# Kernel optimization log

Measured on AMD Instinct MI355X. Metric: run time of the kernel, lower is better.

The kernel has to match this reference:

```python
import jax, jax.numpy as jnp
import numpy as np

N_NODES = 100000
N_EDGES = 500000
HIDDEN = 256


def setup_inputs() -> dict:
    key = jax.random.key(0)
    k_x, k_e, k_w1, k_b1, k_w2, k_b2 = jax.random.split(key, 6)
    x = jax.random.normal(k_x, (N_NODES, HIDDEN), dtype=jnp.float32)
    edge_label_index = jax.random.randint(k_e, (2, N_EDGES), 0, N_NODES, dtype=jnp.int64)
    # fc1: Linear(2*hidden -> hidden); fc2: Linear(hidden -> 1). PyTorch stores W as [out, in].
    bound1 = 1.0 / np.sqrt(2 * HIDDEN)
    W1 = jax.random.uniform(k_w1, (HIDDEN, 2 * HIDDEN), dtype=jnp.float32, minval=-bound1, maxval=bound1)
    b1 = jax.random.uniform(k_b1, (HIDDEN,), dtype=jnp.float32, minval=-bound1, maxval=bound1)
    bound2 = 1.0 / np.sqrt(HIDDEN)
    W2 = jax.random.uniform(k_w2, (1, HIDDEN), dtype=jnp.float32, minval=-bound2, maxval=bound2)
    b2 = jax.random.uniform(k_b2, (1,), dtype=jnp.float32, minval=-bound2, maxval=bound2)
    return {"x": x, "edge_label_index": edge_label_index, "W1": W1, "b1": b1, "W2": W2, "b2": b2}


def reference(x, edge_label_index, W1, b1, W2, b2):
    # Gather endpoint features: [E, H] each
    feat_src = x[edge_label_index[0]]
    feat_dst = x[edge_label_index[1]]
    h = jnp.concatenate([feat_src, feat_dst], axis=1)  # [E, 2H]
    h = jax.nn.relu(h @ W1.T + b1)                      # [E, H]
    out = jax.nn.sigmoid(h @ W2.T + b2)                 # [E, 1]
    return out.reshape(-1)
```

## Files before the change

kernel.cpp:

```cpp
#include <hip/hip_runtime.h>
#include <math.h>

#define NNODES 100000
#define MT     64
#define NTILES 1563
#define NODESP (NTILES * MT)
#define NEDGES 500000
#define HID    256
#define K2     512

typedef _Float16 h8v __attribute__((ext_vector_type(8)));
typedef _Float16 h2v __attribute__((ext_vector_type(2)));
typedef __bf16   bf16x8 __attribute__((ext_vector_type(8)));
typedef float    f32x4  __attribute__((ext_vector_type(4)));

__device__ __forceinline__ unsigned short f2bf(float f) {
    unsigned int u = __float_as_uint(f);
    u += 0x7FFFu + ((u >> 16) & 1u);
    return (unsigned short)(u >> 16);
}
__device__ __forceinline__ float bf2f(unsigned short s) {
    return __uint_as_float(((unsigned int)s) << 16);
}

__global__ void cvt_w1h(const float* __restrict__ W1, _Float16* __restrict__ Bsw) {
    int t = blockIdx.x * 256 + threadIdx.x;
    if (t >= 8 * 32 * 64) return;
    int lane = t & 63, nt = (t >> 6) & 31, kt = t >> 11;
    int j = nt * 16 + (lane & 15);
    int k = kt * 32 + ((lane >> 4) << 3);
    const float* src = W1 + (size_t)(j & 255) * K2 + ((j >> 8) << 8) + k;
    union { _Float16 s[8]; uint4 v; } u;
#pragma unroll
    for (int jj = 0; jj < 8; ++jj) u.s[jj] = (_Float16)src[jj];
    ((uint4*)Bsw)[t] = u.v;
}

__global__ __launch_bounds__(512, 4) void node_gemm3(
    const float* __restrict__ x,
    const _Float16* __restrict__ Bsw,
    const float* __restrict__ b1,
    _Float16* __restrict__ UV)
{
    __shared__ __align__(16) _Float16 Asw[2048 * 8];
    const int tid  = threadIdx.x;
    const int lane = tid & 63;
    const int wave = tid >> 6;
    const int m0   = blockIdx.x * MT;

    uint4* A4 = (uint4*)Asw;
    {
        const int k8 = tid & 31;
        const int mh = tid >> 5;
        const int ktl = k8 >> 2, q = k8 & 3;
#pragma unroll
        for (int i = 0; i < 4; ++i) {
            int m   = i * 16 + mh;
            int row = m0 + m;
            int rl  = row < NNODES ? row : 0;
            const float4* p = (const float4*)(x + (size_t)rl * 256 + k8 * 8);
            float4 a = p[0], b = p[1];
            union { _Float16 s[8]; uint4 v; } u;
            u.s[0] = (_Float16)a.x; u.s[1] = (_Float16)a.y;
            u.s[2] = (_Float16)a.z; u.s[3] = (_Float16)a.w;
            u.s[4] = (_Float16)b.x; u.s[5] = (_Float16)b.y;
            u.s[6] = (_Float16)b.z; u.s[7] = (_Float16)b.w;
            int logical = (ktl << 8) + ((m >> 4) << 6) + (q << 4) + (m & 15);
            A4[logical ^ ktl] = u.v;
        }
    }
    __syncthreads();

    f32x4 acc[4][4] = {};
    const h8v* A8 = (const h8v*)Asw;
    const h8v* B8 = (const h8v*)Bsw;
#pragma unroll
    for (int ks = 0; ks < 8; ++ks) {
        h8v af[4], bfr[4];
#pragma unroll
        for (int mt = 0; mt < 4; ++mt)
            af[mt] = A8[(((ks * 4 + mt) << 6) + lane) ^ ks];
#pragma unroll
        for (int nt = 0; nt < 4; ++nt)
            bfr[nt] = B8[((size_t)(ks * 32 + wave * 4 + nt)) * 64 + lane];
#pragma unroll
        for (int mt = 0; mt < 4; ++mt)
#pragma unroll
            for (int nt = 0; nt < 4; ++nt)
                acc[mt][nt] = __builtin_amdgcn_mfma_f32_16x16x32_f16(
                    af[mt], bfr[nt], acc[mt][nt], 0, 0, 0);
    }

    float b1v[4];
#pragma unroll
    for (int nt = 0; nt < 4; ++nt) {
        int col = wave * 64 + nt * 16 + (lane & 15);
        b1v[nt] = (col < 256) ? b1[col] : 0.0f;
    }
#pragma unroll
    for (int mt = 0; mt < 4; ++mt) {
#pragma unroll
        for (int nt = 0; nt < 4; ++nt) {
            int col = wave * 64 + nt * 16 + (lane & 15);
#pragma unroll
            for (int r = 0; r < 4; ++r) {
                int row = m0 + mt * 16 + ((lane >> 4) << 2) + r;
                UV[(size_t)row * 512 + col] = (_Float16)(acc[mt][nt][r] + b1v[nt]);
            }
        }
    }
}

__global__ __launch_bounds__(256) void edge_out3(
    const _Float16* __restrict__ UV,
    const int* __restrict__ ei,
    const float* __restrict__ W2,
    const float* __restrict__ b2,
    float* __restrict__ out)
{
    const int tid = threadIdx.x;
    const int q   = tid & 31;
    const int g   = tid >> 5;
    const long e  = (long)blockIdx.x * 32 + g * 4;

    int4 s4 = *(const int4*)(ei + e);
    int4 d4 = *(const int4*)(ei + NEDGES + e);

    h2v w2h[4];
    {
        const float4* pw = (const float4*)W2 + q * 2;
        float4 c = pw[0], d = pw[1];
        w2h[0] = h2v{(_Float16)c.x, (_Float16)c.y};
        w2h[1] = h2v{(_Float16)c.z, (_Float16)c.w};
        w2h[2] = h2v{(_Float16)d.x, (_Float16)d.y};
        w2h[3] = h2v{(_Float16)d.z, (_Float16)d.w};
    }

    union U8 { uint4 v; h2v h[4]; };
    const _Float16* up = UV + q * 8;

    U8 uu[4], vv[4];
    uu[0].v = *(const uint4*)(up + (size_t)s4.x * 512);
    vv[0].v = *(const uint4*)(up + (size_t)d4.x * 512 + 256);
    uu[1].v = *(const uint4*)(up + (size_t)s4.y * 512);
    vv[1].v = *(const uint4*)(up + (size_t)d4.y * 512 + 256);
    uu[2].v = *(const uint4*)(up + (size_t)s4.z * 512);
    vv[2].v = *(const uint4*)(up + (size_t)d4.z * 512 + 256);
    uu[3].v = *(const uint4*)(up + (size_t)s4.w * 512);
    vv[3].v = *(const uint4*)(up + (size_t)d4.w * 512 + 256);

    const h2v zz = {(_Float16)0.0f, (_Float16)0.0f};
    float z[4] = {0.f, 0.f, 0.f, 0.f};
#pragma unroll
    for (int ed = 0; ed < 4; ++ed) {
#pragma unroll
        for (int p = 0; p < 4; ++p) {
            h2v h = uu[ed].h[p] + vv[ed].h[p];
            h = __builtin_elementwise_max(h, zz);
            z[ed] = __builtin_amdgcn_fdot2(h, w2h[p], z[ed], false);
        }
    }
#pragma unroll
    for (int m = 1; m < 32; m <<= 1) {
        z[0] += __shfl_xor(z[0], m, 32);
        z[1] += __shfl_xor(z[1], m, 32);
        z[2] += __shfl_xor(z[2], m, 32);
        z[3] += __shfl_xor(z[3], m, 32);
    }
    if (q < 4) {
        float zq = (q == 0) ? z[0] : (q == 1) ? z[1] : (q == 2) ? z[2] : z[3];
        out[e + q] = 1.0f / (1.0f + expf(-(zq + b2[0])));
    }
}

__global__ void cvt_w1_r1(const float* __restrict__ W1, unsigned short* __restrict__ Bsw) {
    int t = blockIdx.x * 256 + threadIdx.x;
    if (t >= 16 * 16 * 64) return;
    int lane = t & 63, nt = (t >> 6) & 15, kt = t >> 10;
    int n = nt * 16 + (lane & 15);
    int k = kt * 32 + ((lane >> 4) << 3);
    const float* src = W1 + (size_t)n * K2 + k;
    union { unsigned short s[8]; uint4 v; } u;
#pragma unroll
    for (int j = 0; j < 8; ++j) u.s[j] = f2bf(src[j]);
    ((uint4*)Bsw)[t] = u.v;
}

__global__ __launch_bounds__(256) void edge_mlp_fb(
    const float* __restrict__ xf, const int* __restrict__ ei,
    const unsigned short* __restrict__ Bsw, const float* __restrict__ b1,
    const float* __restrict__ W2, const float* __restrict__ b2,
    float* __restrict__ out)
{
    __shared__ __align__(16) unsigned short Asw[8 * 4 * 64 * 8];
    __shared__ float es[64];
    const int tid = threadIdx.x, lane = tid & 63, wave = tid >> 6;
    const int e0 = blockIdx.x * 64;
    if (tid < 64) es[tid] = 0.0f;
    f32x4 acc[4][4] = {};
    const bf16x8* A8 = (const bf16x8*)Asw;
    const bf16x8* B8 = (const bf16x8*)Bsw;
    for (int h = 0; h < 2; ++h) {
#pragma unroll
        for (int i = 0; i < 8; ++i) {
            int m = i * 8 + wave * 2 + (lane >> 5);
            int e = e0 + m;
            int ee = (e < NEDGES) ? e : 0;
            int node = ei[(size_t)h * NEDGES + ee];
            int chunk = lane & 31;
            const float4* p = (const float4*)(xf + ((size_t)node << 8) + (chunk << 3));
            float4 a = p[0], bq = p[1];
            union { unsigned short s[8]; uint4 v4; } u;
            u.s[0] = f2bf(a.x);  u.s[1] = f2bf(a.y);  u.s[2] = f2bf(a.z);  u.s[3] = f2bf(a.w);
            u.s[4] = f2bf(bq.x); u.s[5] = f2bf(bq.y); u.s[6] = f2bf(bq.z); u.s[7] = f2bf(bq.w);
            int ktl = chunk >> 2, qq = chunk & 3;
            int u16 = ((ktl * 4 + (m >> 4)) << 6) + (qq << 4) + (m & 15);
            u16 ^= (u16 >> 8) & 7;
            ((uint4*)Asw)[u16] = u.v4;
        }
        __syncthreads();
#pragma unroll
        for (int kt = 0; kt < 8; ++kt) {
            bf16x8 af[4], bfr[4];
#pragma unroll
            for (int mt = 0; mt < 4; ++mt) {
                int u16 = ((kt * 4 + mt) << 6) + lane;
                u16 ^= (u16 >> 8) & 7;
                af[mt] = A8[u16];
            }
#pragma unroll
            for (int nt = 0; nt < 4; ++nt)
                bfr[nt] = B8[(((h * 8 + kt) << 4) + (wave << 2) + nt) * 64 + lane];
#pragma unroll
            for (int mt = 0; mt < 4; ++mt)
#pragma unroll
                for (int nt = 0; nt < 4; ++nt)
                    acc[mt][nt] = __builtin_amdgcn_mfma_f32_16x16x32_bf16(
                        af[mt], bfr[nt], acc[mt][nt], 0, 0, 0);
        }
        __syncthreads();
    }
    float w2v[4], b1v[4];
#pragma unroll
    for (int nt = 0; nt < 4; ++nt) {
        int n = (wave << 6) + (nt << 4) + (lane & 15);
        w2v[nt] = W2[n]; b1v[nt] = b1[n];
    }
#pragma unroll
    for (int mt = 0; mt < 4; ++mt) {
#pragma unroll
        for (int r = 0; r < 4; ++r) {
            float p = 0.0f;
#pragma unroll
            for (int nt = 0; nt < 4; ++nt) {
                float hv = acc[mt][nt][r] + b1v[nt];
                p = fmaf(fmaxf(hv, 0.0f), w2v[nt], p);
            }
            p += __shfl_xor(p, 1, 16);
            p += __shfl_xor(p, 2, 16);
            p += __shfl_xor(p, 4, 16);
            p += __shfl_xor(p, 8, 16);
            if ((lane & 15) == 0)
                atomicAdd(&es[(mt << 4) + ((lane >> 4) << 2) + r], p);
        }
    }
    __syncthreads();
    if (tid < 64) {
        int e = e0 + tid;
        if (e < NEDGES) out[e] = 1.0f / (1.0f + expf(-(es[tid] + b2[0])));
    }
}

extern "C" void kernel_launch(void* const* d_in, const int* in_sizes, int n_in,
                              void* d_out, int out_size, void* d_ws, size_t ws_size,
                              hipStream_t stream) {
    const float* x  = (const float*)d_in[0];
    const int*   ei = (const int*)d_in[1];
    const float* W1 = (const float*)d_in[2];
    const float* b1 = (const float*)d_in[3];
    const float* W2 = (const float*)d_in[4];
    const float* b2 = (const float*)d_in[5];
    float* out = (float*)d_out;

    const size_t BSW_BYTES = 1 << 18;
    const size_t UV_BYTES  = (size_t)NODESP * K2 * 2;
    const size_t NEED_A = BSW_BYTES + UV_BYTES;

    if (ws_size >= NEED_A) {
        _Float16* Bsw = (_Float16*)d_ws;
        _Float16* UV  = (_Float16*)((char*)d_ws + BSW_BYTES);
        cvt_w1h<<<64, 256, 0, stream>>>(W1, Bsw);
        node_gemm3<<<NTILES, 512, 0, stream>>>(x, Bsw, b1, UV);
        edge_out3<<<NEDGES / 32, 256, 0, stream>>>(UV, ei, W2, b2, out);
    } else {
        unsigned short* Bsw = (unsigned short*)d_ws;
        cvt_w1_r1<<<64, 256, 0, stream>>>(W1, Bsw);
        edge_mlp_fb<<<(NEDGES + 63) / 64, 256, 0, stream>>>(x, ei, Bsw, b1, W2, b2, out);
    }
}
```

Baseline: 258.0 us.

## Make node GEMM persistent with register-resident W1 and packed UV stores

The node GEMM becomes a persistent kernel with a fixed grid that loops over row tiles. Each wave keeps its slice of the W1 fragments in registers for the whole run instead of reloading them per tile. The next tile's x rows are staged into shared memory while the current tile's results are written, and UV is written as packed 4-half stores. To keep the edge kernel's dot product consistent with the new interleaved UV column order, W2 is permuted once into a workspace buffer. The cost is heavy register use (occupancy hint drops to 2) and a grid of only 256 blocks, which may underfill the GPU.

Measured after the change: 253.4 us. About the same (-1.8%).

```diff
diff --git a/kernel.cpp b/kernel.cpp
--- a/kernel.cpp
+++ b/kernel.cpp
@@ -8,6 +8,7 @@
 #define NEDGES 500000
 #define HID    256
 #define K2     512
+#define GEMM_GRID 256
 
 typedef _Float16 h8v __attribute__((ext_vector_type(8)));
 typedef _Float16 h2v __attribute__((ext_vector_type(2)));
@@ -18,9 +19,6 @@
     unsigned int u = __float_as_uint(f);
     u += 0x7FFFu + ((u >> 16) & 1u);
     return (unsigned short)(u >> 16);
-}
-__device__ __forceinline__ float bf2f(unsigned short s) {
-    return __uint_as_float(((unsigned int)s) << 16);
 }
 
 __global__ void cvt_w1h(const float* __restrict__ W1, _Float16* __restrict__ Bsw) {
@@ -36,7 +34,13 @@
     ((uint4*)Bsw)[t] = u.v;
 }
 
-__global__ __launch_bounds__(512, 4) void node_gemm3(
+__global__ void cvt_w2p(const float* __restrict__ W2, float* __restrict__ w2p) {
+    int t = threadIdx.x;
+    int i = (t >> 2) & 15, nt = t & 3;
+    w2p[t] = W2[(t & ~63) | (nt * 16 + i)];
+}
+
+__global__ __launch_bounds__(512, 2) void node_gemm4(
     const float* __restrict__ x,
     const _Float16* __restrict__ Bsw,
     const float* __restrict__ b1,
@@ -46,17 +50,33 @@
     const int tid  = threadIdx.x;
     const int lane = tid & 63;
     const int wave = tid >> 6;
-    const int m0   = blockIdx.x * MT;
+
+    const h8v* B8 = (const h8v*)Bsw;
+    h8v barr[8][4];
+#pragma unroll
+    for (int ks = 0; ks < 8; ++ks)
+#pragma unroll
+        for (int nt = 0; nt < 4; ++nt)
+            barr[ks][nt] = B8[((size_t)(ks * 32 + wave * 4 + nt)) * 64 + lane];
+
+    float b1v[4];
+#pragma unroll
+    for (int nt = 0; nt < 4; ++nt) {
+        int col = wave * 64 + nt * 16 + (lane & 15);
+        b1v[nt] = (col < 256) ? b1[col] : 0.0f;
+    }
 
     uint4* A4 = (uint4*)Asw;
-    {
-        const int k8 = tid & 31;
-        const int mh = tid >> 5;
-        const int ktl = k8 >> 2, q = k8 & 3;
+    const h8v* A8 = (const h8v*)Asw;
+    const int k8  = tid & 31;
+    const int mh  = tid >> 5;
+    const int ktl = k8 >> 2, q = k8 & 3;
+
+    auto stage = [&](int tile) {
 #pragma unroll
         for (int i = 0; i < 4; ++i) {
             int m   = i * 16 + mh;
-            int row = m0 + m;
+            int row = tile * MT + m;
             int rl  = row < NNODES ? row : 0;
             const float4* p = (const float4*)(x + (size_t)rl * 256 + k8 * 8);
             float4 a = p[0], b = p[1];
@@ -68,53 +88,61 @@
             int logical = (ktl << 8) + ((m >> 4) << 6) + (q << 4) + (m & 15);
             A4[logical ^ ktl] = u.v;
         }
-    }
+    };
+
+    f32x4 acc[4][4] = {};
+    int tile = blockIdx.x;
+    if (tile >= NTILES) return;
+    stage(tile);
     __syncthreads();
 
-    f32x4 acc[4][4] = {};
-    const h8v* A8 = (const h8v*)Asw;
-    const h8v* B8 = (const h8v*)Bsw;
-#pragma unroll
-    for (int ks = 0; ks < 8; ++ks) {
-        h8v af[4], bfr[4];
+    while (true) {
+#pragma unroll
+        for (int ks = 0; ks < 8; ++ks) {
+            h8v af[4];
+#pragma unroll
+            for (int mt = 0; mt < 4; ++mt)
+                af[mt] = A8[(((ks * 4 + mt) << 6) + lane) ^ ks];
+#pragma unroll
+            for (int mt = 0; mt < 4; ++mt)
+#pragma unroll
+                for (int nt = 0; nt < 4; ++nt)
+                    acc[mt][nt] = __builtin_amdgcn_mfma_f32_16x16x32_f16(
+                        af[mt], barr[ks][nt], acc[mt][nt], 0, 0, 0);
+        }
+        __syncthreads();
+
+        int next = tile + GEMM_GRID;
+        if (next < NTILES) stage(next);
+
+#pragma unroll
+        for (int mt = 0; mt < 4; ++mt) {
+#pragma unroll
+            for (int r = 0; r < 4; ++r) {
+                int row = tile * MT + mt * 16 + ((lane >> 4) << 2) + r;
+                union { _Float16 h[4]; uint2 v; } pk;
+#pragma unroll
+                for (int nt = 0; nt < 4; ++nt)
+                    pk.h[nt] = (_Float16)(acc[mt][nt][r] + b1v[nt]);
+                *(uint2*)(UV + (size_t)row * 512 + wave * 64 + (lane & 15) * 4) = pk.v;
+            }
+        }
 #pragma unroll
         for (int mt = 0; mt < 4; ++mt)
-            af[mt] = A8[(((ks * 4 + mt) << 6) + lane) ^ ks];
-#pragma unroll
-        for (int nt = 0; nt < 4; ++nt)
-            bfr[nt] = B8[((size_t)(ks * 32 + wave * 4 + nt)) * 64 + lane];
-#pragma unroll
-        for (int mt = 0; mt < 4; ++mt)
 #pragma unroll
             for (int nt = 0; nt < 4; ++nt)
-                acc[mt][nt] = __builtin_amdgcn_mfma_f32_16x16x32_f16(
-                    af[mt], bfr[nt], acc[mt][nt], 0, 0, 0);
-    }
-
-    float b1v[4];
-#pragma unroll
-    for (int nt = 0; nt < 4; ++nt) {
-        int col = wave * 64 + nt * 16 + (lane & 15);
-        b1v[nt] = (col < 256) ? b1[col] : 0.0f;
-    }
-#pragma unroll
-    for (int mt = 0; mt < 4; ++mt) {
-#pragma unroll
-        for (int nt = 0; nt < 4; ++nt) {
-            int col = wave * 64 + nt * 16 + (lane & 15);
-#pragma unroll
-            for (int r = 0; r < 4; ++r) {
-                int row = m0 + mt * 16 + ((lane >> 4) << 2) + r;
-                UV[(size_t)row * 512 + col] = (_Float16)(acc[mt][nt][r] + b1v[nt]);
-            }
-        }
-    }
-}
-
-__global__ __launch_bounds__(256) void edge_out3(
+                acc[mt][nt] = f32x4{0.f, 0.f, 0.f, 0.f};
+
+        if (next >= NTILES) break;
+        tile = next;
+        __syncthreads();
+    }
+}
+
+__global__ __launch_bounds__(256) void edge_out4(
     const _Float16* __restrict__ UV,
     const int* __restrict__ ei,
-    const float* __restrict__ W2,
+    const float* __restrict__ w2p,
     const float* __restrict__ b2,
     float* __restrict__ out)
 {
@@ -128,7 +156,7 @@
 
     h2v w2h[4];
     {
-        const float4* pw = (const float4*)W2 + q * 2;
+        const float4* pw = (const float4*)w2p + q * 2;
         float4 c = pw[0], d = pw[1];
         w2h[0] = h2v{(_Float16)c.x, (_Float16)c.y};
         w2h[1] = h2v{(_Float16)c.z, (_Float16)c.w};
@@ -283,15 +311,18 @@
     float* out = (float*)d_out;
 
     const size_t BSW_BYTES = 1 << 18;
+    const size_t W2P_BYTES = 4096;
     const size_t UV_BYTES  = (size_t)NODESP * K2 * 2;
-    const size_t NEED_A = BSW_BYTES + UV_BYTES;
+    const size_t NEED_A = BSW_BYTES + W2P_BYTES + UV_BYTES;
 
     if (ws_size >= NEED_A) {
         _Float16* Bsw = (_Float16*)d_ws;
-        _Float16* UV  = (_Float16*)((char*)d_ws + BSW_BYTES);
+        float*    w2p = (float*)((char*)d_ws + BSW_BYTES);
+        _Float16* UV  = (_Float16*)((char*)d_ws + BSW_BYTES + W2P_BYTES);
         cvt_w1h<<<64, 256, 0, stream>>>(W1, Bsw);
-        node_gemm3<<<NTILES, 512, 0, stream>>>(x, Bsw, b1, UV);
-        edge_out3<<<NEDGES / 32, 256, 0, stream>>>(UV, ei, W2, b2, out);
+        cvt_w2p<<<1, 256, 0, stream>>>(W2, w2p);
+        node_gemm4<<<GEMM_GRID, 512, 0, stream>>>(x, Bsw, b1, UV);
+        edge_out4<<<NEDGES / 32, 256, 0, stream>>>(UV, ei, w2p, b2, out);
     } else {
         unsigned short* Bsw = (unsigned short*)d_ws;
         cvt_w1_r1<<<64, 256, 0, stream>>>(W1, Bsw);
```
